# Kernel optimization log

Measured on AMD Instinct MI355X. Metric: run time of the kernel, lower is better.

Reference implementation:

```python
import jax, jax.numpy as jnp
import numpy as np

MARGIN = 1.0
EPS = 1e-12


def setup_inputs() -> dict:
    key = jax.random.key(0)
    k1, k2, k3 = jax.random.split(key, 3)
    inputs = jax.random.normal(k1, (8192, 128), dtype=jnp.float32)
    targets = jax.random.randint(k2, (8192,), 0, 64, dtype=jnp.int64)
    center = jax.random.normal(k3, (16, 128), dtype=jnp.float32)
    return {"inputs": inputs, "targets": targets, "center": center}


def reference(inputs, targets, center):
    n = inputs.shape[0]
    # pairwise Euclidean distances via ||a||^2 + ||b||^2 - 2 a.b  (matches addmm_ trick)
    sq = jnp.sum(inputs * inputs, axis=1)                      # [n]
    dist2 = sq[:, None] + sq[None, :] - 2.0 * (inputs @ inputs.T)
    dist = jnp.sqrt(jnp.clip(dist2, EPS))                      # [n, n]

    mask = targets[:, None] == targets[None, :]                # same-class mask [n, n]

    # batch-hard mining, fully vectorized (replaces per-row python loops)
    dist_ap = jnp.max(jnp.where(mask, dist, -jnp.inf), axis=1)  # hardest positive
    neg_min = jnp.min(jnp.where(mask, jnp.inf, dist), axis=1)   # hardest negative
    has_neg = jnp.any(~mask, axis=1)
    dist_an = jnp.where(has_neg, neg_min, dist_ap + MARGIN)

    # center augmentation: min over distances to L2-normalized prototypes
    cn = center / jnp.linalg.norm(center, axis=1, keepdims=True)       # [P, d]
    dc = jnp.sqrt(jnp.sum((inputs[:, None, :] - cn[None, :, :]) ** 2, axis=-1))  # [n, P]
    dc = jnp.clip(dc, EPS)
    dist_an = jnp.minimum(dist_an, jnp.min(dc, axis=1))

    # MarginRankingLoss with y=1: mean(relu(dist_ap - dist_an + margin))
    loss = jnp.mean(jnp.maximum(dist_ap - dist_an + MARGIN, 0.0))
    return loss
```

## Files before the change

kernel.cpp:

```cpp
#include <hip/hip_runtime.h>


#define N_ROWS 8192
#define DIM 128
#define KDIM 192
#define ROWB 384
#define NPROTO 16
#define MARGIN_F 1.0f
#define EPS_F 1e-12f
#define BIAS_F 32768.0f

typedef __attribute__((ext_vector_type(8))) short short8;
typedef __attribute__((ext_vector_type(4))) float float4v;
typedef __attribute__((ext_vector_type(4))) unsigned uint4v;

static __device__ __forceinline__ unsigned f2bf(float f) {
  unsigned u = __float_as_uint(f);
  u += 0x7fffu + ((u >> 16) & 1u);
  return u >> 16;
}

static __device__ __forceinline__ void gload_lds16(const void* g, void* l) {
  __builtin_amdgcn_global_load_lds(
      (const __attribute__((address_space(1))) unsigned*)g,
      (__attribute__((address_space(3))) unsigned*)l, 16, 0, 0);
}

__global__ void prep_kernel(const float* __restrict__ x,
                            const float* __restrict__ center,
                            const int* __restrict__ tgt,
                            char* __restrict__ xbf,
                            float* __restrict__ sq,
                            float* __restrict__ mindc,
                            float* __restrict__ out) {
  __shared__ float scn[NPROTO * DIM];
  int tid = threadIdx.x;
  if (blockIdx.x == 0 && tid == 0) out[0] = 0.0f;
  int rloc = tid >> 4, l = tid & 15;
  {
    float v[8];
    float ss = 0.f;
#pragma unroll
    for (int j = 0; j < 8; ++j) {
      v[j] = center[rloc * DIM + l * 8 + j];
      ss += v[j] * v[j];
    }
#pragma unroll
    for (int m = 1; m < 16; m <<= 1) ss += __shfl_xor(ss, m, 64);
    float inv = 1.0f / sqrtf(ss);
#pragma unroll
    for (int j = 0; j < 8; ++j) scn[rloc * DIM + l * 8 + j] = v[j] * inv;
  }
  __syncthreads();

  int row = blockIdx.x * 16 + rloc;
  float4 v0 = ((const float4*)x)[row * 32 + l * 2];
  float4 v1 = ((const float4*)x)[row * 32 + l * 2 + 1];
  float ss = v0.x * v0.x + v0.y * v0.y + v0.z * v0.z + v0.w * v0.w +
             v1.x * v1.x + v1.y * v1.y + v1.z * v1.z + v1.w * v1.w;
  float dots[NPROTO];
#pragma unroll
  for (int p = 0; p < NPROTO; ++p) {
    const float* c = &scn[p * DIM + l * 8];
    dots[p] = v0.x * c[0] + v0.y * c[1] + v0.z * c[2] + v0.w * c[3] +
              v1.x * c[4] + v1.y * c[5] + v1.z * c[6] + v1.w * c[7];
  }
#pragma unroll
  for (int m = 1; m < 16; m <<= 1) {
    ss += __shfl_xor(ss, m, 64);
#pragma unroll
    for (int p = 0; p < NPROTO; ++p) dots[p] += __shfl_xor(dots[p], m, 64);
  }
  uint4 pk;
  pk.x = f2bf(v0.x) | (f2bf(v0.y) << 16);
  pk.y = f2bf(v0.z) | (f2bf(v0.w) << 16);
  pk.z = f2bf(v1.x) | (f2bf(v1.y) << 16);
  pk.w = f2bf(v1.z) | (f2bf(v1.w) << 16);
  *(uint4*)(xbf + (size_t)row * ROWB + l * 16) = pk;
  int cls = tgt[row];
  if (l < 8) {
    unsigned wv = (cls & 1) ? 0xC3000000u : 0x0000C300u;
    uint4 oh;
    oh.x = ((cls >> 1) == (l * 4 + 0)) ? wv : 0u;
    oh.y = ((cls >> 1) == (l * 4 + 1)) ? wv : 0u;
    oh.z = ((cls >> 1) == (l * 4 + 2)) ? wv : 0u;
    oh.w = ((cls >> 1) == (l * 4 + 3)) ? wv : 0u;
    *(uint4*)(xbf + (size_t)row * ROWB + 256 + l * 16) = oh;
  }
  if (l == 0) {
    float mind2 = INFINITY;
#pragma unroll
    for (int p = 0; p < NPROTO; ++p)
      mind2 = fminf(mind2, ss + 1.0f - 2.0f * dots[p]);
    sq[row] = ss;
    mindc[row] = fmaxf(sqrtf(fmaxf(mind2, 0.0f)), EPS_F);
  }
}

__global__ __launch_bounds__(256, 2) void
pairdist_kernel(const char* __restrict__ xbf, const float* __restrict__ sq,
                float* __restrict__ pmax, float* __restrict__ pmin) {
  __shared__ __align__(16) char bl[2][24576];
  const int bid = blockIdx.x;
  const int rg = bid >> 4;
  const int strip = bid & 15;
  const int wave = threadIdx.x >> 6, lane = threadIdx.x & 63;
  const int q = lane >> 4, l16 = lane & 15;
  const int rowbase = rg * 256 + wave * 64;
  const int stripbase = strip * 512;

  const int slot = wave * 64 + lane;
  const char* const srcstrip = xbf + (size_t)stripbase * ROWB;
  int soff[6];
#pragma unroll
  for (int r = 0; r < 6; ++r) {
    int o = r * 4096 + slot * 16;
    int c = o / ROWB;
    soff[r] = c * ROWB + ((o - c * ROWB) ^ ((c & 7) << 4));
  }

  auto stage = [&](int s, char* buf) {
    const char* g = srcstrip + (size_t)s * 24576;
#pragma unroll
    for (int r = 0; r < 6; ++r)
      gload_lds16(g + soff[r], buf + r * 4096 + wave * 1024);
  };

  stage(0, bl[0]);

  short8 a[4][6];
#pragma unroll
  for (int rt = 0; rt < 4; ++rt) {
    const char* ar = xbf + (size_t)(rowbase + rt * 16 + l16) * ROWB + q * 16;
#pragma unroll
    for (int kc = 0; kc < 6; ++kc) a[rt][kc] = *(const short8*)(ar + kc * 64);
#pragma unroll
    for (int kc = 4; kc < 6; ++kc) {
      uint4v u = __builtin_bit_cast(uint4v, a[rt][kc]);
      u ^= 0x80008000u;
      a[rt][kc] = __builtin_bit_cast(short8, u);
    }
  }

  int roffb[6];
#pragma unroll
  for (int kc = 0; kc < 6; ++kc)
    roffb[kc] = (l16 * ROWB + kc * 64 + q * 16) ^ ((l16 & 7) << 4);

  float maxp[16], minn[16];
#pragma unroll
  for (int i = 0; i < 16; ++i) {
    maxp[i] = -INFINITY;
    minn[i] = INFINITY;
  }

#pragma unroll 1
  for (int s = 0; s < 8; ++s) {
    __syncthreads();
    if (s + 1 < 8) stage(s + 1, bl[(s + 1) & 1]);
    const char* cur = bl[s & 1];
    float sqs[4];
#pragma unroll
    for (int ss = 0; ss < 4; ++ss)
      sqs[ss] = sq[stripbase + s * 64 + ss * 16 + l16];
#pragma unroll
    for (int ss = 0; ss < 4; ++ss) {
      const char* bufp = cur + ss * 6144;
      short8 b[6];
#pragma unroll
      for (int kc = 0; kc < 6; ++kc)
        b[kc] = *(const short8*)(bufp + roffb[kc]);
      float4v acc[4];
#pragma unroll
      for (int rt = 0; rt < 4; ++rt) acc[rt] = (float4v){0.f, 0.f, 0.f, 0.f};
#pragma unroll
      for (int kc = 0; kc < 6; ++kc)
#pragma unroll
        for (int rt = 0; rt < 4; ++rt)
          acc[rt] = __builtin_amdgcn_mfma_f32_16x16x32_bf16(a[rt][kc], b[kc],
                                                            acc[rt], 0, 0, 0);
#pragma unroll
      for (int rt = 0; rt < 4; ++rt)
#pragma unroll
        for (int r = 0; r < 4; ++r) {
          float v = fmaf(-2.0f, acc[rt][r], sqs[ss]);
          int idx = rt * 4 + r;
          maxp[idx] = fmaxf(maxp[idx], v);
          minn[idx] = fminf(minn[idx], v);
        }
    }
  }

#pragma unroll
  for (int m = 1; m < 16; m <<= 1)
#pragma unroll
    for (int i = 0; i < 16; ++i) {
      maxp[i] = fmaxf(maxp[i], __shfl_xor(maxp[i], m, 64));
      minn[i] = fminf(minn[i], __shfl_xor(minn[i], m, 64));
    }
  if (l16 == 0) {
    float* pM = pmax + (size_t)strip * N_ROWS + rowbase + q * 4;
    float* pm = pmin + (size_t)strip * N_ROWS + rowbase + q * 4;
#pragma unroll
    for (int rt = 0; rt < 4; ++rt)
#pragma unroll
      for (int r = 0; r < 4; ++r) {
        pM[rt * 16 + r] = maxp[rt * 4 + r];
        pm[rt * 16 + r] = minn[rt * 4 + r];
      }
  }
}

__global__ void finalize_kernel(const float* __restrict__ pmax,
                                const float* __restrict__ pmin,
                                const float* __restrict__ sq,
                                const float* __restrict__ mindc,
                                float* __restrict__ out) {
  __shared__ float wsum[4];
  int i = blockIdx.x * 256 + threadIdx.x;
  float maxv = -INFINITY, minv = INFINITY;
#pragma unroll
  for (int s = 0; s < 16; ++s) {
    maxv = fmaxf(maxv, pmax[s * N_ROWS + i]);
    minv = fminf(minv, pmin[s * N_ROWS + i]);
  }
  float si = sq[i];
  float dap = sqrtf(fmaxf(si + (maxv - BIAS_F), EPS_F));
  float dan = (minv > 16384.0f) ? (dap + MARGIN_F)
                                : sqrtf(fmaxf(si + minv, EPS_F));
  dan = fminf(dan, mindc[i]);
  float c = fmaxf(dap - dan + MARGIN_F, 0.0f) * (1.0f / (float)N_ROWS);
#pragma unroll
  for (int m = 1; m < 64; m <<= 1) c += __shfl_xor(c, m, 64);
  int lane = threadIdx.x & 63, wv = threadIdx.x >> 6;
  if (lane == 0) wsum[wv] = c;
  __syncthreads();
  if (threadIdx.x == 0) atomicAdd(out, wsum[0] + wsum[1] + wsum[2] + wsum[3]);
}

extern "C" void kernel_launch(void* const* d_in, const int* in_sizes, int n_in,
                              void* d_out, int out_size, void* d_ws, size_t ws_size,
                              hipStream_t stream) {
  const float* inputs = (const float*)d_in[0];
  const int* targets = (const int*)d_in[1];
  const float* center = (const float*)d_in[2];
  char* ws = (char*)d_ws;
  char* xbf    = ws;
  float* sq    = (float*)(ws + 3145728);
  float* mindc = (float*)(ws + 3178496);
  float* pmax  = (float*)(ws + 3211264);
  float* pmin  = (float*)(ws + 3735552);
  float* out   = (float*)d_out;

  prep_kernel<<<512, 256, 0, stream>>>(inputs, center, targets, xbf, sq, mindc, out);
  pairdist_kernel<<<512, 256, 0, stream>>>(xbf, sq, pmax, pmin);
  finalize_kernel<<<32, 256, 0, stream>>>(pmax, pmin, sq, mindc, out);
}
```

Baseline: 92.99 us.

## Triple-buffer LDS staging with manual vmcnt waits and stage sq into LDS

Moves the pairwise-distance kernel from double to triple-buffered LDS staging. It prefetches two stages ahead and replaces __syncthreads with explicit s_waitcnt vmcnt plus s_barrier, so global-to-LDS loads overlap more of the MFMA work. The per-column squared norms are now loaded once into LDS instead of re-read from global memory every stage. It also raises MFMA wave priority with s_setprio and relaxes launch_bounds to one block per SIMD. The extra LDS use and lower occupancy hint may reduce concurrency, and the hand-tuned vmcnt counts have to match the number of loads in flight.

```diff
diff --git a/kernel.cpp b/kernel.cpp
--- a/kernel.cpp
+++ b/kernel.cpp
@@ -6,6 +6,7 @@
 #define KDIM 192
 #define ROWB 384
 #define NPROTO 16
+#define NSTRIP 16
 #define MARGIN_F 1.0f
 #define EPS_F 1e-12f
 #define BIAS_F 32768.0f
@@ -97,19 +98,18 @@
   }
 }
 
-__global__ __launch_bounds__(256, 2) void
+__global__ __launch_bounds__(256, 1) void
 pairdist_kernel(const char* __restrict__ xbf, const float* __restrict__ sq,
                 float* __restrict__ pmax, float* __restrict__ pmin) {
-  __shared__ __align__(16) char bl[2][24576];
-  const int bid = blockIdx.x;
-  const int rg = bid >> 4;
-  const int strip = bid & 15;
+  __shared__ __align__(16) char bl[3][24576];
+  __shared__ __align__(16) float sqlds[512];
   const int wave = threadIdx.x >> 6, lane = threadIdx.x & 63;
   const int q = lane >> 4, l16 = lane & 15;
+  const int rg = blockIdx.x >> 4, strip = blockIdx.x & 15;
   const int rowbase = rg * 256 + wave * 64;
   const int stripbase = strip * 512;
 
-  const int slot = wave * 64 + lane;
+  const int slot = threadIdx.x;
   const char* const srcstrip = xbf + (size_t)stripbase * ROWB;
   int soff[6];
 #pragma unroll
@@ -126,8 +126,6 @@
       gload_lds16(g + soff[r], buf + r * 4096 + wave * 1024);
   };
 
-  stage(0, bl[0]);
-
   short8 a[4][6];
 #pragma unroll
   for (int rt = 0; rt < 4; ++rt) {
@@ -141,6 +139,17 @@
       a[rt][kc] = __builtin_bit_cast(short8, u);
     }
   }
+#pragma unroll
+  for (int rt = 0; rt < 4; ++rt)
+#pragma unroll
+    for (int kc = 0; kc < 6; ++kc)
+      asm volatile("" : "+v"(a[rt][kc]));
+
+  if (wave < 2)
+    gload_lds16((const char*)(sq + stripbase) + wave * 1024 + lane * 16,
+                (char*)sqlds + wave * 1024 + lane * 16);
+  stage(0, bl[0]);
+  stage(1, bl[1]);
 
   int roffb[6];
 #pragma unroll
@@ -149,23 +158,20 @@
 
   float maxp[16], minn[16];
 #pragma unroll
-  for (int i = 0; i < 16; ++i) {
-    maxp[i] = -INFINITY;
-    minn[i] = INFINITY;
-  }
+  for (int i = 0; i < 16; ++i) { maxp[i] = -INFINITY; minn[i] = INFINITY; }
+
+  asm volatile("s_waitcnt vmcnt(6)" ::: "memory");
+  __builtin_amdgcn_s_barrier();
+  asm volatile("" ::: "memory");
 
 #pragma unroll 1
   for (int s = 0; s < 8; ++s) {
-    __syncthreads();
-    if (s + 1 < 8) stage(s + 1, bl[(s + 1) & 1]);
-    const char* cur = bl[s & 1];
-    float sqs[4];
-#pragma unroll
-    for (int ss = 0; ss < 4; ++ss)
-      sqs[ss] = sq[stripbase + s * 64 + ss * 16 + l16];
-#pragma unroll
-    for (int ss = 0; ss < 4; ++ss) {
-      const char* bufp = cur + ss * 6144;
+    if (s + 2 < 8) stage(s + 2, bl[(s + 2) % 3]);
+    const char* cur = bl[s % 3];
+#pragma unroll
+    for (int p = 0; p < 4; ++p) {
+      const char* bufp = cur + p * 6144;
+      float sqc = sqlds[s * 64 + p * 16 + l16];
       short8 b[6];
 #pragma unroll
       for (int kc = 0; kc < 6; ++kc)
@@ -173,21 +179,31 @@
       float4v acc[4];
 #pragma unroll
       for (int rt = 0; rt < 4; ++rt) acc[rt] = (float4v){0.f, 0.f, 0.f, 0.f};
+      __builtin_amdgcn_s_setprio(1);
 #pragma unroll
       for (int kc = 0; kc < 6; ++kc)
 #pragma unroll
         for (int rt = 0; rt < 4; ++rt)
           acc[rt] = __builtin_amdgcn_mfma_f32_16x16x32_bf16(a[rt][kc], b[kc],
                                                             acc[rt], 0, 0, 0);
+      __builtin_amdgcn_s_setprio(0);
 #pragma unroll
       for (int rt = 0; rt < 4; ++rt)
 #pragma unroll
         for (int r = 0; r < 4; ++r) {
-          float v = fmaf(-2.0f, acc[rt][r], sqs[ss]);
+          float v = fmaf(-2.0f, acc[rt][r], sqc);
           int idx = rt * 4 + r;
           maxp[idx] = fmaxf(maxp[idx], v);
           minn[idx] = fminf(minn[idx], v);
         }
+    }
+    if (s < 7) {
+      if (s + 2 < 8)
+        asm volatile("s_waitcnt vmcnt(6)" ::: "memory");
+      else
+        asm volatile("s_waitcnt vmcnt(0)" ::: "memory");
+      __builtin_amdgcn_s_barrier();
+      asm volatile("" ::: "memory");
     }
   }
 
@@ -220,7 +236,7 @@
   int i = blockIdx.x * 256 + threadIdx.x;
   float maxv = -INFINITY, minv = INFINITY;
 #pragma unroll
-  for (int s = 0; s < 16; ++s) {
+  for (int s = 0; s < NSTRIP; ++s) {
     maxv = fmaxf(maxv, pmax[s * N_ROWS + i]);
     minv = fminf(minv, pmin[s * N_ROWS + i]);
   }
```

Result: slower. 104.6 us (+12.5%).
